# Kernel tuning notes

Measured on AMD Instinct MI355X. Metric: run time of the kernel, lower is better.

## Reference

```python
import jax, jax.numpy as jnp
import numpy as np
from jax import lax

DN = ('NCHW', 'OIHW', 'NCHW')


def _conv(x, w, b):
    # SAME-padded 3x3 conv; bias broadcast over spatial dims
    y = lax.conv_general_dilated(x, w, (1, 1), 'SAME', dimension_numbers=DN)
    return y + b[None, :, None, None]


def setup_inputs() -> dict:
    key = jax.random.key(0)
    ks = jax.random.split(key, 6)
    B, Cin, Ch, H, W, K = 8, 16, 32, 256, 256, 3
    fan = (Cin + Ch) * K * K
    scale = 1.0 / np.sqrt(fan)
    return {
        'x': jax.random.normal(ks[0], (B, Cin, H, W), jnp.float32),
        'prev': jax.random.normal(ks[1], (B, Ch, H, W), jnp.float32),
        'mask': jax.random.randint(ks[2], (B, 1, H, W), 0, 2, jnp.int32),
        'w_reset': jax.random.normal(ks[3], (Ch, Cin + Ch, K, K), jnp.float32) * scale,
        'b_reset': jnp.zeros((Ch,), jnp.float32),
        'w_update': jax.random.normal(ks[4], (Ch, Cin + Ch, K, K), jnp.float32) * scale,
        'b_update': jnp.zeros((Ch,), jnp.float32),
        'w_out': jax.random.normal(ks[5], (Ch, Cin + Ch, K, K), jnp.float32) * scale,
        'b_out': jnp.zeros((Ch,), jnp.float32),
    }


def reference(x, prev, mask, w_reset, b_reset, w_update, b_update, w_out, b_out):
    # Dense emulation of submanifold sparse ConvGRU: features exist only at
    # active sites (mask==1); convs gather zeros from inactive sites (matching
    # SCN's rule-based gather) and outputs/biases are masked to active sites.
    m = mask.astype(x.dtype)  # [B,1,H,W] active-site indicator
    x = x * m
    prev = prev * m
    stacked = jnp.concatenate([x, prev], axis=1)  # [B, Cin+Ch, H, W]
    update = jax.nn.sigmoid(_conv(stacked, w_update, b_update)) * m
    reset = jax.nn.sigmoid(_conv(stacked, w_reset, b_reset)) * m
    stacked_r = jnp.concatenate([x, prev * reset], axis=1)
    out_inputs = jnp.tanh(_conv(stacked_r, w_out, b_out)) * m
    # new_state = prev*(1-update) + out_inputs*update (zero off active set)
    new_state = prev * (1.0 - update) + out_inputs * update
    return new_state
```

## Files before the change

kernel.cpp:

```cpp
#include <hip/hip_runtime.h>
#include <hip/hip_bf16.h>
#include <math.h>

#define HH 256
#define WW 256
#define CIN 16
#define CHID 32
#define CST 48
#define TS 16
#define HWPIX (HH * WW)

#define SP 48
#define NKS 14

typedef unsigned short u16;
typedef unsigned int u32;
typedef __attribute__((ext_vector_type(8))) short short8;
typedef __attribute__((ext_vector_type(8))) __bf16 bf16x8;
typedef __attribute__((ext_vector_type(4))) float f32x4;
typedef __attribute__((ext_vector_type(4))) unsigned int u32x4;

__device__ __forceinline__ float b2f(u16 h) {
    union { unsigned u; float f; } v; v.u = ((unsigned)h) << 16; return v.f;
}
__device__ __forceinline__ u16 f2b(float f) {
    union { float f; unsigned u; } v; v.f = f;
    unsigned r = v.u + 0x7fffu + ((v.u >> 16) & 1u);
    return (u16)(r >> 16);
}
__device__ __forceinline__ u32 pk2(float a, float bq) {
    u32 r;
    asm("v_cvt_pk_bf16_f32 %0, %1, %2" : "=v"(r) : "v"(a), "v"(bq));
    return r;
}
__device__ __forceinline__ int imin(int a, int b) { return a < b ? a : b; }

__global__ void packb_kernel(const float* __restrict__ wR, const float* __restrict__ wU,
                             const float* __restrict__ wO, u16* __restrict__ pB) {
    int i = blockIdx.x * 256 + threadIdx.x;
    const int TOT = 3 * NKS * 2 * 64 * 8;
    if (i >= TOT) return;
    int conv = i / (NKS * 2 * 64 * 8);
    int r = i - conv * (NKS * 2 * 64 * 8);
    int ks = r / (2 * 64 * 8); r -= ks * (2 * 64 * 8);
    int nf = r / (64 * 8);     r -= nf * (64 * 8);
    int lane = r >> 3, j = r & 7;
    int k = ks * 32 + (lane >> 4) * 8 + j;
    int n = nf * 16 + (lane & 15);
    float val = 0.f;
    if (k < 432) {
        int tap = k / 48, ci = k - tap * 48;
        const float* w = (conv == 0) ? wR : (conv == 1) ? wU : wO;
        val = w[(n * CST + ci) * 9 + tap];
    }
    pB[i] = f2b(val);
}

__global__ __launch_bounds__(256, 4) void convgru_mfma(
    const float* __restrict__ x, const float* __restrict__ prev,
    const int* __restrict__ mask, const u16* __restrict__ pB,
    const float* __restrict__ bR, const float* __restrict__ bU,
    const float* __restrict__ bO, float* __restrict__ out)
{
    __shared__ __align__(16) unsigned char smem[400 * SP * 2];
    __shared__ float smask[400];
    u16* s1 = (u16*)smem;
    float* sEp = (float*)smem;

    const int flat = (blockIdx.z * gridDim.y + blockIdx.y) * gridDim.x + blockIdx.x;
    const int wid  = ((flat & 7) << 8) | (flat >> 3);
    const int b    = wid >> 8;
    const int y0   = ((wid >> 4) & 15) * TS, x0 = (wid & 15) * TS;

    const int tid = threadIdx.x;
    const int w   = tid >> 6;
    const int lane = tid & 63;
    const int run  = lane >> 4;
    const int lo   = lane & 15;

    #pragma unroll
    for (int rp = 0; rp < 2; rp++) {
        int p = rp * 256 + tid;
        bool act = p < 400;
        int pc = act ? p : 399;
        int yy = (pc * 205) >> 12, xx = pc - yy * 20;
        int gy = y0 + yy - 2, gx = x0 + xx - 2;
        bool in = (unsigned)gy < HH && (unsigned)gx < WW;
        int gyc = in ? gy : 0, gxc = in ? gx : 0;
        float mv = in ? (float)mask[(b * HH + gyc) * WW + gxc] : 0.f;
        if (act) {
            smask[pc] = mv;
            const float* xb = x    + (size_t)b * CIN  * HWPIX + gyc * WW + gxc;
            const float* pb = prev + (size_t)b * CHID * HWPIX + gyc * WW + gxc;
            u32* dst = (u32*)&s1[pc * SP];
            #pragma unroll
            for (int g = 0; g < 6; g++) {
                const float* src = (g < 2) ? (xb + g * 8 * HWPIX)
                                           : (pb + (g * 8 - 16) * HWPIX);
                u32x4 w4;
                #pragma unroll
                for (int h = 0; h < 4; h++) {
                    float v0 = src[(2 * h)     * HWPIX] * mv;
                    float v1 = src[(2 * h + 1) * HWPIX] * mv;
                    w4[h] = pk2(v0, v1);
                }
                *(u32x4*)(dst + g * 4) = w4;
            }
        }
    }
    __syncthreads();

    int koff[NKS];
    #pragma unroll
    for (int ks = 0; ks < NKS; ks++) {
        int klin = ks * 4 + run;
        int tap = imin((klin * 43) >> 8, 8);
        int ci  = imin((klin - tap * 6) * 8, 40);
        int ky = (tap * 11) >> 5, kx = tap - ky * 3;
        koff[ks] = (((ky * 20 + kx) * SP) + ci) * 2;
    }

    const char* s1c = (const char*)s1;
    const short8* pB8 = (const short8*)pB;
    const f32x4 z4 = {0.f, 0.f, 0.f, 0.f};
    const int baseU = ((1 + w) * 20 + 1 + lo) * SP * 2;

    f32x4 accU[4][2];
    #pragma unroll
    for (int f = 0; f < 4; f++) { accU[f][0] = z4; accU[f][1] = z4; }
    {
        short8 bp[2][2];
        bp[0][0] = pB8[(1 * NKS + 0) * 128 + lane];
        bp[0][1] = pB8[(1 * NKS + 0) * 128 + 64 + lane];
        bp[1][0] = pB8[(1 * NKS + 1) * 128 + lane];
        bp[1][1] = pB8[(1 * NKS + 1) * 128 + 64 + lane];
        #pragma unroll
        for (int ks = 0; ks < NKS; ks++) {
            short8 b0 = bp[ks & 1][0], b1 = bp[ks & 1][1];
            if (ks + 2 < NKS) {
                bp[ks & 1][0] = pB8[(1 * NKS + ks + 2) * 128 + lane];
                bp[ks & 1][1] = pB8[(1 * NKS + ks + 2) * 128 + 64 + lane];
            }
            const char* ap = s1c + baseU + koff[ks];
            #pragma unroll
            for (int f = 0; f < 4; f++) {
                short8 av = *(const short8*)(ap + f * (4 * 20 * SP * 2));
                bf16x8 a = __builtin_bit_cast(bf16x8, av);
                accU[f][0] = __builtin_amdgcn_mfma_f32_16x16x32_bf16(a, __builtin_bit_cast(bf16x8, b0), accU[f][0], 0, 0, 0);
                accU[f][1] = __builtin_amdgcn_mfma_f32_16x16x32_bf16(a, __builtin_bit_cast(bf16x8, b1), accU[f][1], 0, 0, 0);
            }
        }
    }

    f32x4 accR[6][2];
    #pragma unroll
    for (int f = 0; f < 6; f++) { accR[f][0] = z4; accR[f][1] = z4; }

    int pbase[6];
    #pragma unroll
    for (int f = 0; f < 6; f++) {
        int frag = w + f * 4;
        int idx = imin(frag * 16 + lo, 323);
        int ry = (idx * 57) >> 10;
        int rx = idx - ry * 18;
        pbase[f] = (ry * 20 + rx) * SP * 2;
    }
    {
        short8 bp[2][2];
        bp[0][0] = pB8[(0 * NKS + 0) * 128 + lane];
        bp[0][1] = pB8[(0 * NKS + 0) * 128 + 64 + lane];
        bp[1][0] = pB8[(0 * NKS + 1) * 128 + lane];
        bp[1][1] = pB8[(0 * NKS + 1) * 128 + 64 + lane];
        #pragma unroll
        for (int ks = 0; ks < NKS; ks++) {
            short8 b0 = bp[ks & 1][0], b1 = bp[ks & 1][1];
            if (ks + 2 < NKS) {
                bp[ks & 1][0] = pB8[(0 * NKS + ks + 2) * 128 + lane];
                bp[ks & 1][1] = pB8[(0 * NKS + ks + 2) * 128 + 64 + lane];
            }
            #pragma unroll
            for (int f = 0; f < 6; f++) {
                if (f == 5 && w > 0) continue;
                short8 av = *(const short8*)(s1c + pbase[f] + koff[ks]);
                bf16x8 a = __builtin_bit_cast(bf16x8, av);
                accR[f][0] = __builtin_amdgcn_mfma_f32_16x16x32_bf16(a, __builtin_bit_cast(bf16x8, b0), accR[f][0], 0, 0, 0);
                accR[f][1] = __builtin_amdgcn_mfma_f32_16x16x32_bf16(a, __builtin_bit_cast(bf16x8, b1), accR[f][1], 0, 0, 0);
            }
        }
    }

    unsigned pms[4][4];
    #pragma unroll
    for (int f = 0; f < 4; f++) {
        int py = w + f * 4;
        #pragma unroll
        for (int reg = 0; reg < 4; reg++) {
            int px = run * 4 + reg;
            int base = ((py + 2) * 20 + px + 2) * SP + CIN + lo;
            unsigned a0 = s1[base];
            unsigned a1 = s1[base + 16];
            pms[f][reg] = a0 | (a1 << 16);
        }
    }
    __syncthreads();

    {
        float bRv0 = bR[lo], bRv1 = bR[16 + lo];
        #pragma unroll
        for (int f = 0; f < 6; f++) {
            if (f == 5 && w > 0) continue;
            int frag = w + f * 4;
            #pragma unroll
            for (int reg = 0; reg < 4; reg++) {
                int idx = frag * 16 + run * 4 + reg;
                bool valid = idx < 324;
                int idc = imin(idx, 323);
                int ry = (idc * 57) >> 10, rx = idc - ry * 18;
                int base = ((ry + 1) * 20 + rx + 1) * SP + CIN + lo;
                float z0 = accR[f][0][reg] + bRv0;
                float sg0 = 1.f / (1.f + __expf(-z0));
                float z1 = accR[f][1][reg] + bRv1;
                float sg1 = 1.f / (1.f + __expf(-z1));
                float pm0 = b2f(s1[base]);
                float pm1 = b2f(s1[base + 16]);
                if (valid) {
                    s1[base]      = f2b(pm0 * sg0);
                    s1[base + 16] = f2b(pm1 * sg1);
                }
            }
        }
    }
    __syncthreads();

    f32x4 accO[4][2];
    #pragma unroll
    for (int f = 0; f < 4; f++) { accO[f][0] = z4; accO[f][1] = z4; }
    {
        short8 bp[2][2];
        bp[0][0] = pB8[(2 * NKS + 0) * 128 + lane];
        bp[0][1] = pB8[(2 * NKS + 0) * 128 + 64 + lane];
        bp[1][0] = pB8[(2 * NKS + 1) * 128 + lane];
        bp[1][1] = pB8[(2 * NKS + 1) * 128 + 64 + lane];
        #pragma unroll
        for (int ks = 0; ks < NKS; ks++) {
            short8 b0 = bp[ks & 1][0], b1 = bp[ks & 1][1];
            if (ks + 2 < NKS) {
                bp[ks & 1][0] = pB8[(2 * NKS + ks + 2) * 128 + lane];
                bp[ks & 1][1] = pB8[(2 * NKS + ks + 2) * 128 + 64 + lane];
            }
            const char* ap = s1c + baseU + koff[ks];
            #pragma unroll
            for (int f = 0; f < 4; f++) {
                short8 av = *(const short8*)(ap + f * (4 * 20 * SP * 2));
                bf16x8 a = __builtin_bit_cast(bf16x8, av);
                accO[f][0] = __builtin_amdgcn_mfma_f32_16x16x32_bf16(a, __builtin_bit_cast(bf16x8, b0), accO[f][0], 0, 0, 0);
                accO[f][1] = __builtin_amdgcn_mfma_f32_16x16x32_bf16(a, __builtin_bit_cast(bf16x8, b1), accO[f][1], 0, 0, 0);
            }
        }
    }
    __syncthreads();

    {
        float bUv0 = bU[lo], bUv1 = bU[16 + lo];
        float bOv0 = bO[lo], bOv1 = bO[16 + lo];
        #pragma unroll
        for (int f = 0; f < 4; f++) {
            int py = w + f * 4;
            #pragma unroll
            for (int reg = 0; reg < 4; reg++) {
                int px = run * 4 + reg;
                float mm = smask[(py + 2) * 20 + px + 2];
                unsigned pmw = pms[f][reg];
                #pragma unroll
                for (int nf = 0; nf < 2; nf++) {
                    int c = nf * 16 + lo;
                    float zu = accU[f][nf][reg] + (nf ? bUv1 : bUv0);
                    float uu = mm / (1.f + __expf(-zu));
                    float zo = accO[f][nf][reg] + (nf ? bOv1 : bOv0);
                    float e2 = __expf(2.f * zo);
                    float t = (1.f - 2.f / (e2 + 1.f)) * mm;
                    float pm = b2f((u16)((pmw >> (nf * 16)) & 0xffffu));
                    sEp[c * 260 + py * 16 + px] = pm * (1.f - uu) + t * uu;
                }
            }
        }
    }
    __syncthreads();

    #pragma unroll
    for (int r = 0; r < 8; r++) {
        int i = r * 256 + tid;
        int c = i >> 6;
        int q = (i & 63) * 4;
        f32x4 v = *(const f32x4*)&sEp[c * 260 + q];
        int py = q >> 4, px = q & 15;
        *(f32x4*)&out[((size_t)(b * CHID + c) * HH + y0 + py) * WW + x0 + px] = v;
    }
}

extern "C" void kernel_launch(void* const* d_in, const int* in_sizes, int n_in,
                              void* d_out, int out_size, void* d_ws, size_t ws_size,
                              hipStream_t stream) {
    const float* x       = (const float*)d_in[0];
    const float* prev    = (const float*)d_in[1];
    const int*   mask    = (const int*)d_in[2];
    const float* w_reset = (const float*)d_in[3];
    const float* b_reset = (const float*)d_in[4];
    const float* w_upd   = (const float*)d_in[5];
    const float* b_upd   = (const float*)d_in[6];
    const float* w_out   = (const float*)d_in[7];
    const float* b_out   = (const float*)d_in[8];
    float* out = (float*)d_out;

    u16* pB = (u16*)d_ws;
    const int TOT = 3 * NKS * 2 * 64 * 8;
    packb_kernel<<<(TOT + 255) / 256, 256, 0, stream>>>(w_reset, w_upd, w_out, pB);

    dim3 grid(WW / TS, HH / TS, 8);
    convgru_mfma<<<grid, 256, 0, stream>>>(x, prev, mask, pB,
                                           b_reset, b_upd, b_out, out);
}
```

Baseline: 94.13 us.

## Fuse update-gate conv into reset conv loop over halo fragments

```diff
diff --git a/kernel.cpp b/kernel.cpp
--- a/kernel.cpp
+++ b/kernel.cpp
@@ -120,42 +120,6 @@
         koff[ks] = (((ky * 20 + kx) * SP) + ci) * 2;
     }
 
-    const char* s1c = (const char*)s1;
-    const short8* pB8 = (const short8*)pB;
-    const f32x4 z4 = {0.f, 0.f, 0.f, 0.f};
-    const int baseU = ((1 + w) * 20 + 1 + lo) * SP * 2;
-
-    f32x4 accU[4][2];
-    #pragma unroll
-    for (int f = 0; f < 4; f++) { accU[f][0] = z4; accU[f][1] = z4; }
-    {
-        short8 bp[2][2];
-        bp[0][0] = pB8[(1 * NKS + 0) * 128 + lane];
-        bp[0][1] = pB8[(1 * NKS + 0) * 128 + 64 + lane];
-        bp[1][0] = pB8[(1 * NKS + 1) * 128 + lane];
-        bp[1][1] = pB8[(1 * NKS + 1) * 128 + 64 + lane];
-        #pragma unroll
-        for (int ks = 0; ks < NKS; ks++) {
-            short8 b0 = bp[ks & 1][0], b1 = bp[ks & 1][1];
-            if (ks + 2 < NKS) {
-                bp[ks & 1][0] = pB8[(1 * NKS + ks + 2) * 128 + lane];
-                bp[ks & 1][1] = pB8[(1 * NKS + ks + 2) * 128 + 64 + lane];
-            }
-            const char* ap = s1c + baseU + koff[ks];
-            #pragma unroll
-            for (int f = 0; f < 4; f++) {
-                short8 av = *(const short8*)(ap + f * (4 * 20 * SP * 2));
-                bf16x8 a = __builtin_bit_cast(bf16x8, av);
-                accU[f][0] = __builtin_amdgcn_mfma_f32_16x16x32_bf16(a, __builtin_bit_cast(bf16x8, b0), accU[f][0], 0, 0, 0);
-                accU[f][1] = __builtin_amdgcn_mfma_f32_16x16x32_bf16(a, __builtin_bit_cast(bf16x8, b1), accU[f][1], 0, 0, 0);
-            }
-        }
-    }
-
-    f32x4 accR[6][2];
-    #pragma unroll
-    for (int f = 0; f < 6; f++) { accR[f][0] = z4; accR[f][1] = z4; }
-
     int pbase[6];
     #pragma unroll
     for (int f = 0; f < 6; f++) {
@@ -165,45 +129,52 @@
         int rx = idx - ry * 18;
         pbase[f] = (ry * 20 + rx) * SP * 2;
     }
-    {
-        short8 bp[2][2];
-        bp[0][0] = pB8[(0 * NKS + 0) * 128 + lane];
-        bp[0][1] = pB8[(0 * NKS + 0) * 128 + 64 + lane];
-        bp[1][0] = pB8[(0 * NKS + 1) * 128 + lane];
-        bp[1][1] = pB8[(0 * NKS + 1) * 128 + 64 + lane];
+
+    const char* s1c = (const char*)s1;
+    const short8* pB8 = (const short8*)pB;
+    const f32x4 z4 = {0.f, 0.f, 0.f, 0.f};
+
+    f32x4 accR[6][2], accU[6][2];
+    #pragma unroll
+    for (int f = 0; f < 6; f++) {
+        accR[f][0] = z4; accR[f][1] = z4;
+        accU[f][0] = z4; accU[f][1] = z4;
+    }
+    {
+        short8 bpR[2][2], bpU[2][2];
+        bpR[0][0] = pB8[(0 * NKS + 0) * 128 + lane];
+        bpR[0][1] = pB8[(0 * NKS + 0) * 128 + 64 + lane];
+        bpU[0][0] = pB8[(1 * NKS + 0) * 128 + lane];
+        bpU[0][1] = pB8[(1 * NKS + 0) * 128 + 64 + lane];
+        bpR[1][0] = pB8[(0 * NKS + 1) * 128 + lane];
+        bpR[1][1] = pB8[(0 * NKS + 1) * 128 + 64 + lane];
+        bpU[1][0] = pB8[(1 * NKS + 1) * 128 + lane];
+        bpU[1][1] = pB8[(1 * NKS + 1) * 128 + 64 + lane];
         #pragma unroll
         for (int ks = 0; ks < NKS; ks++) {
-            short8 b0 = bp[ks & 1][0], b1 = bp[ks & 1][1];
+            short8 b0R = bpR[ks & 1][0], b1R = bpR[ks & 1][1];
+            short8 b0U = bpU[ks & 1][0], b1U = bpU[ks & 1][1];
             if (ks + 2 < NKS) {
-                bp[ks & 1][0] = pB8[(0 * NKS + ks + 2) * 128 + lane];
-                bp[ks & 1][1] = pB8[(0 * NKS + ks + 2) * 128 + 64 + lane];
+                bpR[ks & 1][0] = pB8[(0 * NKS + ks + 2) * 128 + lane];
+                bpR[ks & 1][1] = pB8[(0 * NKS + ks + 2) * 128 + 64 + lane];
+                bpU[ks & 1][0] = pB8[(1 * NKS + ks + 2) * 128 + lane];
+                bpU[ks & 1][1] = pB8[(1 * NKS + ks + 2) * 128 + 64 + lane];
             }
             #pragma unroll
             for (int f = 0; f < 6; f++) {
                 if (f == 5 && w > 0) continue;
                 short8 av = *(const short8*)(s1c + pbase[f] + koff[ks]);
                 bf16x8 a = __builtin_bit_cast(bf16x8, av);
-                accR[f][0] = __builtin_amdgcn_mfma_f32_16x16x32_bf16(a, __builtin_bit_cast(bf16x8, b0), accR[f][0], 0, 0, 0);
-                accR[f][1] = __builtin_amdgcn_mfma_f32_16x16x32_bf16(a, __builtin_bit_cast(bf16x8, b1), accR[f][1], 0, 0, 0);
-            }
-        }
-    }
-
-    unsigned pms[4][4];
-    #pragma unroll
-    for (int f = 0; f < 4; f++) {
-        int py = w + f * 4;
-        #pragma unroll
-        for (int reg = 0; reg < 4; reg++) {
-            int px = run * 4 + reg;
-            int base = ((py + 2) * 20 + px + 2) * SP + CIN + lo;
-            unsigned a0 = s1[base];
-            unsigned a1 = s1[base + 16];
-            pms[f][reg] = a0 | (a1 << 16);
-        }
-    }
-    __syncthreads();
-
+                accR[f][0] = __builtin_amdgcn_mfma_f32_16x16x32_bf16(a, __builtin_bit_cast(bf16x8, b0R), accR[f][0], 0, 0, 0);
+                accR[f][1] = __builtin_amdgcn_mfma_f32_16x16x32_bf16(a, __builtin_bit_cast(bf16x8, b1R), accR[f][1], 0, 0, 0);
+                accU[f][0] = __builtin_amdgcn_mfma_f32_16x16x32_bf16(a, __builtin_bit_cast(bf16x8, b0U), accU[f][0], 0, 0, 0);
+                accU[f][1] = __builtin_amdgcn_mfma_f32_16x16x32_bf16(a, __builtin_bit_cast(bf16x8, b1U), accU[f][1], 0, 0, 0);
+            }
+        }
+    }
+    __syncthreads();
+
+    unsigned pms[6][4];
     {
         float bRv0 = bR[lo], bRv1 = bR[16 + lo];
         #pragma unroll
@@ -217,24 +188,25 @@
                 int idc = imin(idx, 323);
                 int ry = (idc * 57) >> 10, rx = idc - ry * 18;
                 int base = ((ry + 1) * 20 + rx + 1) * SP + CIN + lo;
+                unsigned pm0 = s1[base];
+                unsigned pm1 = s1[base + 16];
+                pms[f][reg] = pm0 | (pm1 << 16);
                 float z0 = accR[f][0][reg] + bRv0;
                 float sg0 = 1.f / (1.f + __expf(-z0));
                 float z1 = accR[f][1][reg] + bRv1;
                 float sg1 = 1.f / (1.f + __expf(-z1));
-                float pm0 = b2f(s1[base]);
-                float pm1 = b2f(s1[base + 16]);
                 if (valid) {
-                    s1[base]      = f2b(pm0 * sg0);
-                    s1[base + 16] = f2b(pm1 * sg1);
+                    s1[base]      = f2b(b2f((u16)pm0) * sg0);
+                    s1[base + 16] = f2b(b2f((u16)(pm1)) * sg1);
                 }
             }
         }
     }
     __syncthreads();
 
-    f32x4 accO[4][2];
-    #pragma unroll
-    for (int f = 0; f < 4; f++) { accO[f][0] = z4; accO[f][1] = z4; }
+    f32x4 accO[6][2];
+    #pragma unroll
+    for (int f = 0; f < 6; f++) { accO[f][0] = z4; accO[f][1] = z4; }
     {
         short8 bp[2][2];
         bp[0][0] = pB8[(2 * NKS + 0) * 128 + lane];
@@ -248,10 +220,10 @@
                 bp[ks & 1][0] = pB8[(2 * NKS + ks + 2) * 128 + lane];
                 bp[ks & 1][1] = pB8[(2 * NKS + ks + 2) * 128 + 64 + lane];
             }
-            const char* ap = s1c + baseU + koff[ks];
-            #pragma unroll
-            for (int f = 0; f < 4; f++) {
-                short8 av = *(const short8*)(ap + f * (4 * 20 * SP * 2));
+            #pragma unroll
+            for (int f = 0; f < 6; f++) {
+                if (f == 5 && w > 0) continue;
+                short8 av = *(const short8*)(s1c + pbase[f] + koff[ks]);
                 bf16x8 a = __builtin_bit_cast(bf16x8, av);
                 accO[f][0] = __builtin_amdgcn_mfma_f32_16x16x32_bf16(a, __builtin_bit_cast(bf16x8, b0), accO[f][0], 0, 0, 0);
                 accO[f][1] = __builtin_amdgcn_mfma_f32_16x16x32_bf16(a, __builtin_bit_cast(bf16x8, b1), accO[f][1], 0, 0, 0);
@@ -264,13 +236,18 @@
         float bUv0 = bU[lo], bUv1 = bU[16 + lo];
         float bOv0 = bO[lo], bOv1 = bO[16 + lo];
         #pragma unroll
-        for (int f = 0; f < 4; f++) {
-            int py = w + f * 4;
+        for (int f = 0; f < 6; f++) {
+            if (f == 5 && w > 0) continue;
+            int frag = w + f * 4;
             #pragma unroll
             for (int reg = 0; reg < 4; reg++) {
-                int px = run * 4 + reg;
-                float mm = smask[(py + 2) * 20 + px + 2];
+                int idx = frag * 16 + run * 4 + reg;
+                int idc = imin(idx, 323);
+                int ry = (idc * 57) >> 10, rx = idc - ry * 18;
+                bool valid = (idx < 324) & (ry >= 1) & (ry < 17) & (rx >= 1) & (rx < 17);
+                float mm = smask[(ry + 1) * 20 + rx + 1];
                 unsigned pmw = pms[f][reg];
+                int py = ry - 1, px = rx - 1;
                 #pragma unroll
                 for (int nf = 0; nf < 2; nf++) {
                     int c = nf * 16 + lo;
@@ -280,7 +257,7 @@
                     float e2 = __expf(2.f * zo);
                     float t = (1.f - 2.f / (e2 + 1.f)) * mm;
                     float pm = b2f((u16)((pmw >> (nf * 16)) & 0xffffu));
-                    sEp[c * 260 + py * 16 + px] = pm * (1.f - uu) + t * uu;
+                    if (valid) sEp[c * 260 + py * 16 + px] = pm * (1.f - uu) + t * uu;
                 }
             }
         }
```

Result: slower. 295.6 us (+214.1%).

## Enlarge tile to 32x16 with 512-thread blocks, pad LDS stride, raise MFMA priority

Applied to the files above, without the earlier changes.

```diff
diff --git a/kernel.cpp b/kernel.cpp
--- a/kernel.cpp
+++ b/kernel.cpp
@@ -7,11 +7,18 @@
 #define CIN 16
 #define CHID 32
 #define CST 48
-#define TS 16
 #define HWPIX (HH * WW)
 
-#define SP 48
+#define TSX 32
+#define TSY 16
+#define HX 36
+#define HY 20
+#define NPX (HX * HY)
+#define SP 56
 #define NKS 14
+#define RNX 34
+#define RNY 18
+#define RPOS (RNX * RNY)
 
 typedef unsigned short u16;
 typedef unsigned int u32;
@@ -56,40 +63,42 @@
     pB[i] = f2b(val);
 }
 
-__global__ __launch_bounds__(256, 4) void convgru_mfma(
+__global__ __launch_bounds__(512, 4) void convgru_mfma(
     const float* __restrict__ x, const float* __restrict__ prev,
     const int* __restrict__ mask, const u16* __restrict__ pB,
     const float* __restrict__ bR, const float* __restrict__ bU,
     const float* __restrict__ bO, float* __restrict__ out)
 {
-    __shared__ __align__(16) unsigned char smem[400 * SP * 2];
-    __shared__ float smask[400];
-    u16* s1 = (u16*)smem;
-    float* sEp = (float*)smem;
+    __shared__ __align__(16) u16 s1[NPX * SP];
+    __shared__ unsigned char smask8[NPX];
+    float* sEp = (float*)s1;
 
     const int flat = (blockIdx.z * gridDim.y + blockIdx.y) * gridDim.x + blockIdx.x;
-    const int wid  = ((flat & 7) << 8) | (flat >> 3);
-    const int b    = wid >> 8;
-    const int y0   = ((wid >> 4) & 15) * TS, x0 = (wid & 15) * TS;
+    const int wid  = ((flat & 7) << 7) | (flat >> 3);
+    const int b    = wid >> 7;
+    const int y0   = ((wid >> 3) & 15) * TSY;
+    const int x0   = (wid & 7) * TSX;
 
     const int tid = threadIdx.x;
-    const int w   = tid >> 6;
+    const int w    = tid >> 6;
     const int lane = tid & 63;
     const int run  = lane >> 4;
     const int lo   = lane & 15;
 
     #pragma unroll
     for (int rp = 0; rp < 2; rp++) {
-        int p = rp * 256 + tid;
-        bool act = p < 400;
-        int pc = act ? p : 399;
-        int yy = (pc * 205) >> 12, xx = pc - yy * 20;
+        int p = rp * 512 + tid;
+        bool act = p < NPX;
+        int pc = act ? p : (NPX - 1);
+        int yy = (pc * 911) >> 15;
+        int xx = pc - yy * HX;
         int gy = y0 + yy - 2, gx = x0 + xx - 2;
         bool in = (unsigned)gy < HH && (unsigned)gx < WW;
         int gyc = in ? gy : 0, gxc = in ? gx : 0;
-        float mv = in ? (float)mask[(b * HH + gyc) * WW + gxc] : 0.f;
+        int mi = in ? mask[(b * HH + gyc) * WW + gxc] : 0;
+        float mv = (float)mi;
         if (act) {
-            smask[pc] = mv;
+            smask8[pc] = (unsigned char)mi;
             const float* xb = x    + (size_t)b * CIN  * HWPIX + gyc * WW + gxc;
             const float* pb = prev + (size_t)b * CHID * HWPIX + gyc * WW + gxc;
             u32* dst = (u32*)&s1[pc * SP];
@@ -117,13 +126,14 @@
         int tap = imin((klin * 43) >> 8, 8);
         int ci  = imin((klin - tap * 6) * 8, 40);
         int ky = (tap * 11) >> 5, kx = tap - ky * 3;
-        koff[ks] = (((ky * 20 + kx) * SP) + ci) * 2;
+        koff[ks] = (((ky * HX + kx) * SP) + ci) * 2;
     }
 
     const char* s1c = (const char*)s1;
     const short8* pB8 = (const short8*)pB;
     const f32x4 z4 = {0.f, 0.f, 0.f, 0.f};
-    const int baseU = ((1 + w) * 20 + 1 + lo) * SP * 2;
+    const int baseU = (((2 * w) + 1) * HX + 1 + lo) * SP * 2;
+    const int fOffB[4] = {0, 16 * SP * 2, HX * SP * 2, (HX + 16) * SP * 2};
 
     f32x4 accU[4][2];
     #pragma unroll
@@ -142,28 +152,30 @@
                 bp[ks & 1][1] = pB8[(1 * NKS + ks + 2) * 128 + 64 + lane];
             }
             const char* ap = s1c + baseU + koff[ks];
+            __builtin_amdgcn_s_setprio(1);
             #pragma unroll
             for (int f = 0; f < 4; f++) {
-                short8 av = *(const short8*)(ap + f * (4 * 20 * SP * 2));
+                short8 av = *(const short8*)(ap + fOffB[f]);
                 bf16x8 a = __builtin_bit_cast(bf16x8, av);
                 accU[f][0] = __builtin_amdgcn_mfma_f32_16x16x32_bf16(a, __builtin_bit_cast(bf16x8, b0), accU[f][0], 0, 0, 0);
                 accU[f][1] = __builtin_amdgcn_mfma_f32_16x16x32_bf16(a, __builtin_bit_cast(bf16x8, b1), accU[f][1], 0, 0, 0);
             }
-        }
-    }
-
-    f32x4 accR[6][2];
-    #pragma unroll
-    for (int f = 0; f < 6; f++) { accR[f][0] = z4; accR[f][1] = z4; }
-
-    int pbase[6];
-    #pragma unroll
-    for (int f = 0; f < 6; f++) {
-        int frag = w + f * 4;
-        int idx = imin(frag * 16 + lo, 323);
-        int ry = (idx * 57) >> 10;
-        int rx = idx - ry * 18;
-        pbase[f] = (ry * 20 + rx) * SP * 2;
+            __builtin_amdgcn_s_setprio(0);
+        }
+    }
+
+    f32x4 accR[5][2];
+    #pragma unroll
+    for (int f = 0; f < 5; f++) { accR[f][0] = z4; accR[f][1] = z4; }
+
+    int pbase[5];
+    #pragma unroll
+    for (int f = 0; f < 5; f++) {
+        int frag = w + f * 8;
+        int idx = imin(frag * 16 + lo, RPOS - 1);
+        int ry = (idx * 241) >> 13;
+        int rx = idx - ry * RNX;
+        pbase[f] = (ry * HX + rx) * SP * 2;
     }
     {
         short8 bp[2][2];
@@ -178,25 +190,28 @@
                 bp[ks & 1][0] = pB8[(0 * NKS + ks + 2) * 128 + lane];
                 bp[ks & 1][1] = pB8[(0 * NKS + ks + 2) * 128 + 64 + lane];
             }
-            #pragma unroll
-            for (int f = 0; f < 6; f++) {
-                if (f == 5 && w > 0) continue;
+            __builtin_amdgcn_s_setprio(1);
+            #pragma unroll
+            for (int f = 0; f < 5; f++) {
+                if (f == 4 && w == 7) continue;
                 short8 av = *(const short8*)(s1c + pbase[f] + koff[ks]);
                 bf16x8 a = __builtin_bit_cast(bf16x8, av);
                 accR[f][0] = __builtin_amdgcn_mfma_f32_16x16x32_bf16(a, __builtin_bit_cast(bf16x8, b0), accR[f][0], 0, 0, 0);
                 accR[f][1] = __builtin_amdgcn_mfma_f32_16x16x32_bf16(a, __builtin_bit_cast(bf16x8, b1), accR[f][1], 0, 0, 0);
             }
+            __builtin_amdgcn_s_setprio(0);
         }
     }
 
     unsigned pms[4][4];
     #pragma unroll
     for (int f = 0; f < 4; f++) {
-        int py = w + f * 4;
+        int row = 2 * w + (f >> 1);
+        int xh  = (f & 1) * 16;
         #pragma unroll
         for (int reg = 0; reg < 4; reg++) {
-            int px = run * 4 + reg;
-            int base = ((py + 2) * 20 + px + 2) * SP + CIN + lo;
+            int px = xh + run * 4 + reg;
+            int base = ((row + 2) * HX + px + 2) * SP + CIN + lo;
             unsigned a0 = s1[base];
             unsigned a1 = s1[base + 16];
             pms[f][reg] = a0 | (a1 << 16);
@@ -207,16 +222,16 @@
     {
         float bRv0 = bR[lo], bRv1 = bR[16 + lo];
         #pragma unroll
-        for (int f = 0; f < 6; f++) {
-            if (f == 5 && w > 0) continue;
-            int frag = w + f * 4;
+        for (int f = 0; f < 5; f++) {
+            if (f == 4 && w == 7) continue;
+            int frag = w + f * 8;
             #pragma unroll
             for (int reg = 0; reg < 4; reg++) {
                 int idx = frag * 16 + run * 4 + reg;
-                bool valid = idx < 324;
-                int idc = imin(idx, 323);
-                int ry = (idc * 57) >> 10, rx = idc - ry * 18;
-                int base = ((ry + 1) * 20 + rx + 1) * SP + CIN + lo;
+                bool valid = idx < RPOS;
+                int idc = imin(idx, RPOS - 1);
+                int ry = (idc * 241) >> 13, rx = idc - ry * RNX;
+                int base = ((ry + 1) * HX + rx + 1) * SP + CIN + lo;
                 float z0 = accR[f][0][reg] + bRv0;
                 float sg0 = 1.f / (1.f + __expf(-z0));
                 float z1 = accR[f][1][reg] + bRv1;
@@ -249,13 +264,15 @@
                 bp[ks & 1][1] = pB8[(2 * NKS + ks + 2) * 128 + 64 + lane];
             }
             const char* ap = s1c + baseU + koff[ks];
+            __builtin_amdgcn_s_setprio(1);
             #pragma unroll
             for (int f = 0; f < 4; f++) {
-                short8 av = *(const short8*)(ap + f * (4 * 20 * SP * 2));
+                short8 av = *(const short8*)(ap + fOffB[f]);
                 bf16x8 a = __builtin_bit_cast(bf16x8, av);
                 accO[f][0] = __builtin_amdgcn_mfma_f32_16x16x32_bf16(a, __builtin_bit_cast(bf16x8, b0), accO[f][0], 0, 0, 0);
                 accO[f][1] = __builtin_amdgcn_mfma_f32_16x16x32_bf16(a, __builtin_bit_cast(bf16x8, b1), accO[f][1], 0, 0, 0);
             }
+            __builtin_amdgcn_s_setprio(0);
         }
     }
     __syncthreads();
@@ -265,11 +282,12 @@
         float bOv0 = bO[lo], bOv1 = bO[16 + lo];
         #pragma unroll
         for (int f = 0; f < 4; f++) {
-            int py = w + f * 4;
+            int row = 2 * w + (f >> 1);
+            int xh  = (f & 1) * 16;
             #pragma unroll
             for (int reg = 0; reg < 4; reg++) {
-                int px = run * 4 + reg;
-                float mm = smask[(py + 2) * 20 + px + 2];
+                int px = xh + run * 4 + reg;
+                float mm = (float)smask8[(row + 2) * HX + px + 2];
                 unsigned pmw = pms[f][reg];
                 #pragma unroll
                 for (int nf = 0; nf < 2; nf++) {
@@ -280,7 +298,7 @@
                     float e2 = __expf(2.f * zo);
                     float t = (1.f - 2.f / (e2 + 1.f)) * mm;
                     float pm = b2f((u16)((pmw >> (nf * 16)) & 0xffffu));
-                    sEp[c * 260 + py * 16 + px] = pm * (1.f - uu) + t * uu;
+                    sEp[c * 520 + row * TSX + px] = pm * (1.f - uu) + t * uu;
                 }
             }
         }
@@ -289,12 +307,12 @@
 
     #pragma unroll
     for (int r = 0; r < 8; r++) {
-        int i = r * 256 + tid;
-        int c = i >> 6;
-        int q = (i & 63) * 4;
-        f32x4 v = *(const f32x4*)&sEp[c * 260 + q];
-        int py = q >> 4, px = q & 15;
-        *(f32x4*)&out[((size_t)(b * CHID + c) * HH + y0 + py) * WW + x0 + px] = v;
+        int i = r * 512 + tid;
+        int c = i >> 7;
+        int q = (i & 127) * 4;
+        f32x4 v = *(const f32x4*)&sEp[c * 520 + q];
+        int row = q >> 5, col = q & 31;
+        *(f32x4*)&out[((size_t)(b * CHID + c) * HH + y0 + row) * WW + x0 + col] = v;
     }
 }
 
@@ -316,7 +334,7 @@
     const int TOT = 3 * NKS * 2 * 64 * 8;
     packb_kernel<<<(TOT + 255) / 256, 256, 0, stream>>>(w_reset, w_upd, w_out, pB);
 
-    dim3 grid(WW / TS, HH / TS, 8);
-    convgru_mfma<<<grid, 256, 0, stream>>>(x, prev, mask, pB,
+    dim3 grid(WW / TSX, HH / TSY, 8);
+    convgru_mfma<<<grid, 512, 0, stream>>>(x, prev, mask, pB,
                                            b_reset, b_upd, b_out, out);
 }
```

Measured after the change: 88.02 us. 1.07x faster.
